# Kernel tuning notes

Hardware: AMD Instinct MI355X
Metric: run time of the kernel (lower is better)

Reference implementation:

```python
import jax, jax.numpy as jnp
import numpy as np
from functools import partial

D, H, W = 32, 256, 256   # grid_size (D, H, W)
V = 40000                # number of active voxels
C_IN, C_OUT = 16, 32
K = 3                    # kernel size
P = 32                   # max_points per voxel
EPS = 1e-5               # BatchNorm eps


def setup_inputs() -> dict:
    key = jax.random.key(0)
    k1, k2, k3, k4 = jax.random.split(key, 4)
    voxels = jax.random.normal(k1, (V, C_IN, P), dtype=jnp.float32)
    lin = jax.random.choice(k2, D * H * W, (V,), replace=False)
    d = (lin // (H * W)).astype(jnp.int32)
    h = ((lin // W) % H).astype(jnp.int32)
    w = (lin % W).astype(jnp.int32)
    indices = jnp.stack([w, h, d], axis=1)  # columns are (w, h, d) per original usage
    conv_w = jax.random.normal(k3, (C_OUT, C_IN, K, K, K), dtype=jnp.float32) * 0.05
    conv_b = jax.random.normal(k4, (C_OUT,), dtype=jnp.float32) * 0.05
    gamma = jnp.ones((C_OUT,), dtype=jnp.float32)
    beta = jnp.zeros((C_OUT,), dtype=jnp.float32)
    return {"voxels": voxels, "indices": indices, "conv_w": conv_w,
            "conv_b": conv_b, "gamma": gamma, "beta": beta, "batch_size": 1}


def reference(voxels, indices, conv_w, conv_b, gamma, beta, batch_size):
    # voxel features: mean over points  [V, C]
    feats = voxels.mean(axis=2)
    w_i, h_i, d_i = indices[:, 0], indices[:, 1], indices[:, 2]
    # original: batch_mask = indices[:,0] >= 0, plus per-dim bounds check
    valid = ((w_i >= 0) & (w_i < W) & (h_i >= 0) & (h_i < H) & (d_i >= 0) & (d_i < D))
    d_s = jnp.where(valid, d_i, D)  # route invalid rows out-of-bounds -> dropped
    # fused scatter replacing the python per-voxel loop; [D, H, W, C]
    grid = jnp.zeros((D, H, W, C_IN), dtype=voxels.dtype).at[d_s, h_i, w_i].set(
        feats, mode="drop")
    # same scatter is written into every batch slice in the original
    dense = jnp.broadcast_to(jnp.transpose(grid, (3, 0, 1, 2))[None],
                             (batch_size, C_IN, D, H, W))
    # Conv3d, padding = K//2 (SAME)
    out = jax.lax.conv_general_dilated(
        dense, conv_w, window_strides=(1, 1, 1), padding=[(K // 2, K // 2)] * 3,
        dimension_numbers=("NCDHW", "OIDHW", "NCDHW"))
    out = out + conv_b[None, :, None, None, None]
    # BatchNorm3d (training-mode batch statistics, biased variance)
    mean = out.mean(axis=(0, 2, 3, 4), keepdims=True)
    var = out.var(axis=(0, 2, 3, 4), keepdims=True)
    out = (out - mean) * jax.lax.rsqrt(var + EPS)
    out = out * gamma[None, :, None, None, None] + beta[None, :, None, None, None]
    return jax.nn.relu(out)
```

## Files before the change

kernel.cpp:

```cpp
#include <hip/hip_runtime.h>

#define D_   32
#define H_   256
#define W_   256
#define HW_  (H_ * W_)
#define DHW_ (D_ * H_ * W_)
#define V_   40000
#define CIN  16
#define COUT 32
#define P_   32
#define EPS_ 1e-5f

#define TD 2
#define TH 8
#define TW 32
#define NTX (W_ / TW)
#define NTY (H_ / TH)
#define NTZ (D_ / TD)
#define NT  (NTX * NTY * NTZ)
#define TPOS (TD * TH * TW)
#define OH 8
#define NQ (COUT / OH)
#define TROW 9
#define TCT 512
#define SSLOT 64
#define VBLK ((V_ + 255) / 256)
#define WTN  (NQ * 27 * 4 * OH)
#define WTBLK ((WTN + 255) / 256)

__global__ void tap_count_kernel(const int* __restrict__ idxs, int* __restrict__ tapcnt,
                                 const float* __restrict__ conv_w, float4* __restrict__ wt4) {
    int b = blockIdx.x;
    if (b >= VBLK) {
        int n = (b - VBLK) * 256 + threadIdx.x;
        if (n < WTN) {
            int oo = n & 7;
            int jj = (n >> 3) & 3;
            int m  = n >> 5;
            int k  = m % 27;
            int quarter = m / 27;
            int o = quarter * OH + oo;
            float4 wv;
            wv.x = conv_w[(o * CIN + 4 * jj + 0) * 27 + k];
            wv.y = conv_w[(o * CIN + 4 * jj + 1) * 27 + k];
            wv.z = conv_w[(o * CIN + 4 * jj + 2) * 27 + k];
            wv.w = conv_w[(o * CIN + 4 * jj + 3) * 27 + k];
            wt4[n] = wv;
        }
        return;
    }
    int v = b * 256 + threadIdx.x;
    if (v >= V_) return;
    int w = idxs[3 * v], h = idxs[3 * v + 1], d = idxs[3 * v + 2];
    if (!((unsigned)w < W_ && (unsigned)h < H_ && (unsigned)d < D_)) return;
    int dlo = max(d - 1, 0), dhi = min(d + 1, D_ - 1);
    int hlo = max(h - 1, 0), hhi = min(h + 1, H_ - 1);
    int wlo = max(w - 1, 0), whi = min(w + 1, W_ - 1);
    for (int tz = dlo / TD; tz <= dhi / TD; ++tz) {
        int zl = max(dlo, tz * TD), zh = min(dhi, tz * TD + TD - 1);
        for (int ty = hlo / TH; ty <= hhi / TH; ++ty) {
            int yl = max(hlo, ty * TH), yh = min(hhi, ty * TH + TH - 1);
            for (int tx = wlo / TW; tx <= whi / TW; ++tx) {
                int xl = max(wlo, tx * TW), xh = min(whi, tx * TW + TW - 1);
                int cnt = (zh - zl + 1) * (yh - yl + 1) * (xh - xl + 1);
                atomicAdd(&tapcnt[tz * NTY * NTX + ty * NTX + tx], cnt);
            }
        }
    }
}

__global__ void scan_kernel(const int* __restrict__ counts, int* __restrict__ starts,
                            int* __restrict__ cursor) {
    __shared__ int part[256];
    int t = threadIdx.x;
    int base = t * 16;
    int s = 0;
    for (int j = 0; j < 16; ++j) s += counts[base + j];
    part[t] = s;
    __syncthreads();
    for (int off = 1; off < 256; off <<= 1) {
        int val = part[t];
        int add = (t >= off) ? part[t - off] : 0;
        __syncthreads();
        part[t] = val + add;
        __syncthreads();
    }
    int run = (t > 0) ? part[t - 1] : 0;
    for (int j = 0; j < 16; ++j) {
        starts[base + j] = run;
        cursor[base + j] = run;
        run += counts[base + j];
    }
}

__global__ void tap_fill_kernel(const int* __restrict__ idxs, int* __restrict__ cursor,
                                int* __restrict__ tapbuf) {
    int v = blockIdx.x * 256 + threadIdx.x;
    if (v >= V_) return;
    int w = idxs[3 * v], h = idxs[3 * v + 1], d = idxs[3 * v + 2];
    if (!((unsigned)w < W_ && (unsigned)h < H_ && (unsigned)d < D_)) return;
    int dlo = max(d - 1, 0), dhi = min(d + 1, D_ - 1);
    int hlo = max(h - 1, 0), hhi = min(h + 1, H_ - 1);
    int wlo = max(w - 1, 0), whi = min(w + 1, W_ - 1);
    for (int tz = dlo / TD; tz <= dhi / TD; ++tz) {
        int zl = max(dlo, tz * TD), zh = min(dhi, tz * TD + TD - 1);
        for (int ty = hlo / TH; ty <= hhi / TH; ++ty) {
            int yl = max(hlo, ty * TH), yh = min(hhi, ty * TH + TH - 1);
            for (int tx = wlo / TW; tx <= whi / TW; ++tx) {
                int xl = max(wlo, tx * TW), xh = min(whi, tx * TW + TW - 1);
                int cnt = (zh - zl + 1) * (yh - yl + 1) * (xh - xl + 1);
                int p = atomicAdd(&cursor[tz * NTY * NTX + ty * NTX + tx], cnt);
                for (int dq = zl; dq <= zh; ++dq)
                    for (int hq = yl; hq <= yh; ++hq)
                        for (int wq = xl; wq <= xh; ++wq) {
                            int k = ((d - dq + 1) * 3 + (h - hq + 1)) * 3 + (w - wq + 1);
                            int pos = ((dq & (TD - 1)) * TH + (hq & (TH - 1))) * TW
                                    + (wq & (TW - 1));
                            tapbuf[p++] = (v << 14) | (k << 9) | pos;
                        }
            }
        }
    }
}

__global__ void featpack_kernel(const float* __restrict__ vox, float4* __restrict__ feats4) {
    int idx = blockIdx.x * 256 + threadIdx.x;
    if (idx >= V_ * 4) return;
    int v = idx >> 2, q = idx & 3;
    const float* base = vox + ((size_t)v * CIN + 4 * q) * P_;
    float m[4];
#pragma unroll
    for (int c = 0; c < 4; ++c) {
        const float4* p = (const float4*)(base + c * P_);
        float s = 0.f;
#pragma unroll
        for (int j = 0; j < P_ / 4; ++j) {
            float4 t = p[j];
            s += t.x + t.y + t.z + t.w;
        }
        m[c] = s * (1.0f / (float)P_);
    }
    feats4[v * 4 + q] = make_float4(m[0], m[1], m[2], m[3]);
}

__global__ void __launch_bounds__(TCT, 8) tile_conv_kernel(
    const float4* __restrict__ feats4, const float4* __restrict__ wt4,
    const int* __restrict__ tapstart, const int* __restrict__ tapcnt,
    const int* __restrict__ tapbuf, float* __restrict__ stats,
    float* __restrict__ out)
{
    __shared__ float  tile[TPOS * TROW];
    __shared__ float4 wsm4[27 * 4 * OH];
    __shared__ float  wsum[8][OH], wsq[8][OH];

    int t = threadIdx.x;
    int tile_id = blockIdx.x;
    int quarter = blockIdx.y;
    int gs = tapstart[tile_id];
    int nt = tapcnt[tile_id];
    int tx = tile_id % NTX, ty = (tile_id / NTX) % NTY, tz = tile_id / (NTX * NTY);
    int w0 = tx * TW, h0 = ty * TH, d0 = tz * TD;
    int obase = quarter * OH;

    for (int j = t; j < TPOS * TROW / 4; j += TCT)
        ((float4*)tile)[j] = make_float4(0, 0, 0, 0);
    for (int j = t; j < 27 * 4 * OH; j += TCT)
        wsm4[j] = wt4[quarter * (27 * 4 * OH) + j];
    __syncthreads();

    int oo = t & 7;
    int slot = t >> 3;
    int j = slot;
    if (j < nt) {
        unsigned tap = (unsigned)tapbuf[gs + j];
        const float4* fp = feats4 + (size_t)(tap >> 14) * 4;
        float4 f0 = fp[0], f1 = fp[1], f2 = fp[2], f3 = fp[3];
        while (true) {
            int jn = j + 64;
            bool more = jn < nt;
            unsigned tapn = 0u;
            float4 g0, g1, g2, g3;
            if (more) {
                tapn = (unsigned)tapbuf[gs + jn];
                const float4* gp = feats4 + (size_t)(tapn >> 14) * 4;
                g0 = gp[0]; g1 = gp[1]; g2 = gp[2]; g3 = gp[3];
            }
            int pos = tap & 511;
            int k = (tap >> 9) & 31;
            const float4* wp = &wsm4[(k * 4) * OH + oo];
            float4 q0 = wp[0], q1 = wp[8], q2 = wp[16], q3 = wp[24];
            float acc = q0.x * f0.x + q0.y * f0.y + q0.z * f0.z + q0.w * f0.w
                      + q1.x * f1.x + q1.y * f1.y + q1.z * f1.z + q1.w * f1.w
                      + q2.x * f2.x + q2.y * f2.y + q2.z * f2.z + q2.w * f2.w
                      + q3.x * f3.x + q3.y * f3.y + q3.z * f3.z + q3.w * f3.w;
            atomicAdd(&tile[pos * TROW + oo], acc);
            if (!more) break;
            tap = tapn; f0 = g0; f1 = g1; f2 = g2; f3 = g3; j = jn;
        }
    }
    __syncthreads();

    float s1 = 0.f, s2 = 0.f;
    for (int p = slot; p < TPOS; p += 64) {
        float sv = tile[p * TROW + oo];
        s1 += sv;
        s2 += sv * sv;
    }
    s1 += __shfl_xor(s1, 8);  s2 += __shfl_xor(s2, 8);
    s1 += __shfl_xor(s1, 16); s2 += __shfl_xor(s2, 16);
    s1 += __shfl_xor(s1, 32); s2 += __shfl_xor(s2, 32);
    int wave = t >> 6, lane = t & 63;
    if (lane < OH) { wsum[wave][lane] = s1; wsq[wave][lane] = s2; }

    int wl = t & 31;
    for (int r = t >> 5; r < OH * TD * TH; r += 16) {
        int oo2 = r >> 4;
        int rem = r & 15;
        int pos = rem * TW + wl;
        int dl = rem >> 3, hl = rem & 7;
        out[(size_t)(obase + oo2) * DHW_ + (size_t)(d0 + dl) * HW_ +
            (size_t)(h0 + hl) * W_ + (w0 + wl)] = tile[pos * TROW + oo2];
    }
    __syncthreads();
    if (t < OH) {
        float a = 0.f, b = 0.f;
#pragma unroll
        for (int wv = 0; wv < 8; ++wv) { a += wsum[wv][t]; b += wsq[wv][t]; }
        int sl = tile_id & (SSLOT - 1);
        atomicAdd(&stats[(obase + t) * SSLOT + sl], a);
        atomicAdd(&stats[COUT * SSLOT + (obase + t) * SSLOT + sl], b);
    }
}

__global__ void finalize_kernel(const float* __restrict__ stats,
                                const float* __restrict__ gamma,
                                const float* __restrict__ beta,
                                float* __restrict__ mi) {
    int t = threadIdx.x;
    if (t < COUT) {
        float m1 = 0.f, m2 = 0.f;
        for (int s = 0; s < SSLOT; ++s) {
            m1 += stats[t * SSLOT + s];
            m2 += stats[COUT * SSLOT + t * SSLOT + s];
        }
        float n = (float)DHW_;
        m1 /= n;
        m2 /= n;
        float var = fmaxf(m2 - m1 * m1, 0.f);
        float inv = rsqrtf(var + EPS_);
        float A = gamma[t] * inv;
        mi[t] = A;
        mi[COUT + t] = -m1 * A + beta[t];
    }
}

__global__ void norm_kernel(float* __restrict__ out, const float* __restrict__ mi) {
    int idx4 = blockIdx.x * 256 + threadIdx.x;
    int c = idx4 >> 19;
    float A = mi[c], B = mi[COUT + c];
    float4 x = ((const float4*)out)[idx4];
    x.x = fmaxf(x.x * A + B, 0.f);
    x.y = fmaxf(x.y * A + B, 0.f);
    x.z = fmaxf(x.z * A + B, 0.f);
    x.w = fmaxf(x.w * A + B, 0.f);
    ((float4*)out)[idx4] = x;
}

extern "C" void kernel_launch(void* const* d_in, const int* in_sizes, int n_in,
                              void* d_out, int out_size, void* d_ws, size_t ws_size,
                              hipStream_t stream) {
    const float* voxels  = (const float*)d_in[0];
    const int*   indices = (const int*)  d_in[1];
    const float* conv_w  = (const float*)d_in[2];
    const float* gamma   = (const float*)d_in[4];
    const float* beta    = (const float*)d_in[5];
    float* out = (float*)d_out;

    float4* wt4      = (float4*)d_ws;
    float*  stats    = (float*)(wt4 + WTN);
    float*  mi       = stats + 2 * COUT * SSLOT;
    int*    tapcnt   = (int*)(mi + 2 * COUT);
    int*    tapstart = tapcnt + NT;
    int*    tapcur   = tapstart + NT;
    float4* feats4   = (float4*)(tapcur + NT);
    int*    tapbuf   = (int*)(feats4 + (size_t)V_ * 4);

    hipMemsetAsync(tapcnt, 0, NT * sizeof(int), stream);
    hipMemsetAsync(stats, 0, 2 * COUT * SSLOT * sizeof(float), stream);

    tap_count_kernel<<<VBLK + WTBLK, 256, 0, stream>>>(indices, tapcnt, conv_w, wt4);
    scan_kernel<<<1, 256, 0, stream>>>(tapcnt, tapstart, tapcur);
    tap_fill_kernel<<<VBLK, 256, 0, stream>>>(indices, tapcur, tapbuf);
    featpack_kernel<<<(V_ * 4 + 255) / 256, 256, 0, stream>>>(voxels, feats4);

    dim3 grid(NT, NQ);
    tile_conv_kernel<<<grid, TCT, 0, stream>>>(feats4, wt4, tapstart, tapcnt, tapbuf,
                                               stats, out);
    finalize_kernel<<<1, 64, 0, stream>>>(stats, gamma, beta, mi);

    const int n4 = COUT * DHW_ / 4;
    norm_kernel<<<n4 / 256, 256, 0, stream>>>(out, mi);
}
```

Measured before the change: 664.0 us.

## Merge prep kernels, loop output quarters in-block, fuse finalize into norm

Folds tap counting, weight packing and feature averaging into one prep kernel. The stats zeroing moves into the scan kernel, and the BN finalize step is merged into the norm kernel, which cuts launch count. The conv kernel now loops over the four output-channel quarters inside one block and caches the tile's tap list in shared memory, so taps are not re-read per quarter. It also drops the software prefetch of the next tap, computes stats with per-wave shuffles during the output store, and adds more global atomics.

Result: slower. 811.4 us (+22.2%).

```diff
diff --git a/kernel.cpp b/kernel.cpp
--- a/kernel.cpp
+++ b/kernel.cpp
@@ -24,15 +24,41 @@
 #define TROW 9
 #define TCT 512
 #define SSLOT 64
+#define TAPC 640
 #define VBLK ((V_ + 255) / 256)
 #define WTN  (NQ * 27 * 4 * OH)
 #define WTBLK ((WTN + 255) / 256)
-
-__global__ void tap_count_kernel(const int* __restrict__ idxs, int* __restrict__ tapcnt,
-                                 const float* __restrict__ conv_w, float4* __restrict__ wt4) {
+#define FPBLK ((V_ * 4 + 255) / 256)
+
+__global__ void prep_kernel(const int* __restrict__ idxs, int* __restrict__ tapcnt,
+                            const float* __restrict__ conv_w, float4* __restrict__ wt4,
+                            const float* __restrict__ vox, float4* __restrict__ feats4) {
     int b = blockIdx.x;
-    if (b >= VBLK) {
-        int n = (b - VBLK) * 256 + threadIdx.x;
+    int t = threadIdx.x;
+    if (b < VBLK) {
+        int v = b * 256 + t;
+        if (v >= V_) return;
+        int w = idxs[3 * v], h = idxs[3 * v + 1], d = idxs[3 * v + 2];
+        if (!((unsigned)w < W_ && (unsigned)h < H_ && (unsigned)d < D_)) return;
+        int dlo = max(d - 1, 0), dhi = min(d + 1, D_ - 1);
+        int hlo = max(h - 1, 0), hhi = min(h + 1, H_ - 1);
+        int wlo = max(w - 1, 0), whi = min(w + 1, W_ - 1);
+        for (int tz = dlo / TD; tz <= dhi / TD; ++tz) {
+            int zl = max(dlo, tz * TD), zh = min(dhi, tz * TD + TD - 1);
+            for (int ty = hlo / TH; ty <= hhi / TH; ++ty) {
+                int yl = max(hlo, ty * TH), yh = min(hhi, ty * TH + TH - 1);
+                for (int tx = wlo / TW; tx <= whi / TW; ++tx) {
+                    int xl = max(wlo, tx * TW), xh = min(whi, tx * TW + TW - 1);
+                    int cnt = (zh - zl + 1) * (yh - yl + 1) * (xh - xl + 1);
+                    atomicAdd(&tapcnt[tz * NTY * NTX + ty * NTX + tx], cnt);
+                }
+            }
+        }
+        return;
+    }
+    b -= VBLK;
+    if (b < WTBLK) {
+        int n = b * 256 + t;
         if (n < WTN) {
             int oo = n & 7;
             int jj = (n >> 3) & 3;
@@ -49,30 +75,30 @@
         }
         return;
     }
-    int v = b * 256 + threadIdx.x;
-    if (v >= V_) return;
-    int w = idxs[3 * v], h = idxs[3 * v + 1], d = idxs[3 * v + 2];
-    if (!((unsigned)w < W_ && (unsigned)h < H_ && (unsigned)d < D_)) return;
-    int dlo = max(d - 1, 0), dhi = min(d + 1, D_ - 1);
-    int hlo = max(h - 1, 0), hhi = min(h + 1, H_ - 1);
-    int wlo = max(w - 1, 0), whi = min(w + 1, W_ - 1);
-    for (int tz = dlo / TD; tz <= dhi / TD; ++tz) {
-        int zl = max(dlo, tz * TD), zh = min(dhi, tz * TD + TD - 1);
-        for (int ty = hlo / TH; ty <= hhi / TH; ++ty) {
-            int yl = max(hlo, ty * TH), yh = min(hhi, ty * TH + TH - 1);
-            for (int tx = wlo / TW; tx <= whi / TW; ++tx) {
-                int xl = max(wlo, tx * TW), xh = min(whi, tx * TW + TW - 1);
-                int cnt = (zh - zl + 1) * (yh - yl + 1) * (xh - xl + 1);
-                atomicAdd(&tapcnt[tz * NTY * NTX + ty * NTX + tx], cnt);
-            }
-        }
-    }
+    b -= WTBLK;
+    int idx = b * 256 + t;
+    int v = idx >> 2, q = idx & 3;
+    const float* base = vox + ((size_t)v * CIN + 4 * q) * P_;
+    float m[4];
+#pragma unroll
+    for (int c = 0; c < 4; ++c) {
+        const float4* p = (const float4*)(base + c * P_);
+        float s = 0.f;
+#pragma unroll
+        for (int j = 0; j < P_ / 4; ++j) {
+            float4 tv = p[j];
+            s += tv.x + tv.y + tv.z + tv.w;
+        }
+        m[c] = s * (1.0f / (float)P_);
+    }
+    feats4[v * 4 + q] = make_float4(m[0], m[1], m[2], m[3]);
 }
 
 __global__ void scan_kernel(const int* __restrict__ counts, int* __restrict__ starts,
-                            int* __restrict__ cursor) {
+                            int* __restrict__ cursor, float* __restrict__ stats) {
     __shared__ int part[256];
     int t = threadIdx.x;
+    for (int j = t; j < 2 * COUT * SSLOT; j += 256) stats[j] = 0.f;
     int base = t * 16;
     int s = 0;
     for (int j = 0; j < 16; ++j) s += counts[base + j];
@@ -123,26 +149,6 @@
     }
 }
 
-__global__ void featpack_kernel(const float* __restrict__ vox, float4* __restrict__ feats4) {
-    int idx = blockIdx.x * 256 + threadIdx.x;
-    if (idx >= V_ * 4) return;
-    int v = idx >> 2, q = idx & 3;
-    const float* base = vox + ((size_t)v * CIN + 4 * q) * P_;
-    float m[4];
-#pragma unroll
-    for (int c = 0; c < 4; ++c) {
-        const float4* p = (const float4*)(base + c * P_);
-        float s = 0.f;
-#pragma unroll
-        for (int j = 0; j < P_ / 4; ++j) {
-            float4 t = p[j];
-            s += t.x + t.y + t.z + t.w;
-        }
-        m[c] = s * (1.0f / (float)P_);
-    }
-    feats4[v * 4 + q] = make_float4(m[0], m[1], m[2], m[3]);
-}
-
 __global__ void __launch_bounds__(TCT, 8) tile_conv_kernel(
     const float4* __restrict__ feats4, const float4* __restrict__ wt4,
     const int* __restrict__ tapstart, const int* __restrict__ tapcnt,
@@ -151,42 +157,40 @@
 {
     __shared__ float  tile[TPOS * TROW];
     __shared__ float4 wsm4[27 * 4 * OH];
-    __shared__ float  wsum[8][OH], wsq[8][OH];
+    __shared__ int    taps_l[TAPC];
 
     int t = threadIdx.x;
     int tile_id = blockIdx.x;
-    int quarter = blockIdx.y;
     int gs = tapstart[tile_id];
     int nt = tapcnt[tile_id];
     int tx = tile_id % NTX, ty = (tile_id / NTX) % NTY, tz = tile_id / (NTX * NTY);
     int w0 = tx * TW, h0 = ty * TH, d0 = tz * TD;
-    int obase = quarter * OH;
-
-    for (int j = t; j < TPOS * TROW / 4; j += TCT)
-        ((float4*)tile)[j] = make_float4(0, 0, 0, 0);
-    for (int j = t; j < 27 * 4 * OH; j += TCT)
-        wsm4[j] = wt4[quarter * (27 * 4 * OH) + j];
-    __syncthreads();
-
-    int oo = t & 7;
-    int slot = t >> 3;
-    int j = slot;
-    if (j < nt) {
-        unsigned tap = (unsigned)tapbuf[gs + j];
-        const float4* fp = feats4 + (size_t)(tap >> 14) * 4;
-        float4 f0 = fp[0], f1 = fp[1], f2 = fp[2], f3 = fp[3];
-        while (true) {
-            int jn = j + 64;
-            bool more = jn < nt;
-            unsigned tapn = 0u;
-            float4 g0, g1, g2, g3;
-            if (more) {
-                tapn = (unsigned)tapbuf[gs + jn];
-                const float4* gp = feats4 + (size_t)(tapn >> 14) * 4;
-                g0 = gp[0]; g1 = gp[1]; g2 = gp[2]; g3 = gp[3];
-            }
+    int sl = tile_id & (SSLOT - 1);
+
+    int ntl = min(nt, TAPC);
+    for (int j = t; j < ntl; j += TCT) taps_l[j] = tapbuf[gs + j];
+
+    int oo = t & 7, slot = t >> 3;
+    int wl = t & 31, rem = t >> 5;
+    size_t outb = (size_t)(d0 + (rem >> 3)) * HW_ + (size_t)(h0 + (rem & 7)) * W_
+                + (size_t)(w0 + wl);
+    int posD = (rem * TW + wl) * TROW;
+
+    for (int qq = 0; qq < NQ; ++qq) {
+        int obase = qq * OH;
+        for (int j = t; j < TPOS * TROW / 4; j += TCT)
+            ((float4*)tile)[j] = make_float4(0, 0, 0, 0);
+        for (int j = t; j < 27 * 4 * OH; j += TCT)
+            wsm4[j] = wt4[qq * (27 * 4 * OH) + j];
+        __syncthreads();
+
+        for (int j = slot; j < nt; j += 64) {
+            unsigned tap = (unsigned)((j < TAPC) ? taps_l[j] : tapbuf[gs + j]);
             int pos = tap & 511;
             int k = (tap >> 9) & 31;
+            int src = tap >> 14;
+            const float4* fp = feats4 + (size_t)src * 4;
+            float4 f0 = fp[0], f1 = fp[1], f2 = fp[2], f3 = fp[3];
             const float4* wp = &wsm4[(k * 4) * OH + oo];
             float4 q0 = wp[0], q1 = wp[8], q2 = wp[16], q3 = wp[24];
             float acc = q0.x * f0.x + q0.y * f0.y + q0.z * f0.z + q0.w * f0.w
@@ -194,76 +198,70 @@
                       + q2.x * f2.x + q2.y * f2.y + q2.z * f2.z + q2.w * f2.w
                       + q3.x * f3.x + q3.y * f3.y + q3.z * f3.z + q3.w * f3.w;
             atomicAdd(&tile[pos * TROW + oo], acc);
-            if (!more) break;
-            tap = tapn; f0 = g0; f1 = g1; f2 = g2; f3 = g3; j = jn;
+        }
+        __syncthreads();
+
+        for (int i = 0; i < OH; ++i) {
+            float v = tile[posD + i];
+            out[(size_t)(obase + i) * DHW_ + outb] = v;
+            float a = v, bb = v * v;
+            a += __shfl_xor(a, 1);  bb += __shfl_xor(bb, 1);
+            a += __shfl_xor(a, 2);  bb += __shfl_xor(bb, 2);
+            a += __shfl_xor(a, 4);  bb += __shfl_xor(bb, 4);
+            a += __shfl_xor(a, 8);  bb += __shfl_xor(bb, 8);
+            a += __shfl_xor(a, 16); bb += __shfl_xor(bb, 16);
+            a += __shfl_xor(a, 32); bb += __shfl_xor(bb, 32);
+            if ((t & 63) == 0) {
+                atomicAdd(&stats[(obase + i) * SSLOT + sl], a);
+                atomicAdd(&stats[COUT * SSLOT + (obase + i) * SSLOT + sl], bb);
+            }
+        }
+        __syncthreads();
+    }
+}
+
+__global__ void __launch_bounds__(256) norm_kernel(float* __restrict__ out,
+                                                   const float* __restrict__ stats,
+                                                   const float* __restrict__ gamma,
+                                                   const float* __restrict__ beta) {
+    __shared__ float sAB[2];
+    int t = threadIdx.x;
+    int bid = blockIdx.x;
+    int c = bid >> 7;
+    if (t < 64) {
+        float a = stats[c * SSLOT + t];
+        float b = stats[COUT * SSLOT + c * SSLOT + t];
+        a += __shfl_xor(a, 1);  b += __shfl_xor(b, 1);
+        a += __shfl_xor(a, 2);  b += __shfl_xor(b, 2);
+        a += __shfl_xor(a, 4);  b += __shfl_xor(b, 4);
+        a += __shfl_xor(a, 8);  b += __shfl_xor(b, 8);
+        a += __shfl_xor(a, 16); b += __shfl_xor(b, 16);
+        a += __shfl_xor(a, 32); b += __shfl_xor(b, 32);
+        if (t == 0) {
+            float n = (float)DHW_;
+            float m1 = a / n, m2 = b / n;
+            float var = fmaxf(m2 - m1 * m1, 0.f);
+            float inv = rsqrtf(var + EPS_);
+            float A = gamma[c] * inv;
+            sAB[0] = A;
+            sAB[1] = -m1 * A + beta[c];
         }
     }
     __syncthreads();
-
-    float s1 = 0.f, s2 = 0.f;
-    for (int p = slot; p < TPOS; p += 64) {
-        float sv = tile[p * TROW + oo];
-        s1 += sv;
-        s2 += sv * sv;
-    }
-    s1 += __shfl_xor(s1, 8);  s2 += __shfl_xor(s2, 8);
-    s1 += __shfl_xor(s1, 16); s2 += __shfl_xor(s2, 16);
-    s1 += __shfl_xor(s1, 32); s2 += __shfl_xor(s2, 32);
-    int wave = t >> 6, lane = t & 63;
-    if (lane < OH) { wsum[wave][lane] = s1; wsq[wave][lane] = s2; }
-
-    int wl = t & 31;
-    for (int r = t >> 5; r < OH * TD * TH; r += 16) {
-        int oo2 = r >> 4;
-        int rem = r & 15;
-        int pos = rem * TW + wl;
-        int dl = rem >> 3, hl = rem & 7;
-        out[(size_t)(obase + oo2) * DHW_ + (size_t)(d0 + dl) * HW_ +
-            (size_t)(h0 + hl) * W_ + (w0 + wl)] = tile[pos * TROW + oo2];
-    }
-    __syncthreads();
-    if (t < OH) {
-        float a = 0.f, b = 0.f;
+    float A = sAB[0], B = sAB[1];
+    const int CH4 = DHW_ / 4;
+    int base4 = c * CH4 + (bid & 127) * (CH4 / 128);
+    float4* o4 = (float4*)out;
 #pragma unroll
-        for (int wv = 0; wv < 8; ++wv) { a += wsum[wv][t]; b += wsq[wv][t]; }
-        int sl = tile_id & (SSLOT - 1);
-        atomicAdd(&stats[(obase + t) * SSLOT + sl], a);
-        atomicAdd(&stats[COUT * SSLOT + (obase + t) * SSLOT + sl], b);
-    }
-}
-
-__global__ void finalize_kernel(const float* __restrict__ stats,
-                                const float* __restrict__ gamma,
-                                const float* __restrict__ beta,
-                                float* __restrict__ mi) {
-    int t = threadIdx.x;
-    if (t < COUT) {
-        float m1 = 0.f, m2 = 0.f;
-        for (int s = 0; s < SSLOT; ++s) {
-            m1 += stats[t * SSLOT + s];
-            m2 += stats[COUT * SSLOT + t * SSLOT + s];
-        }
-        float n = (float)DHW_;
-        m1 /= n;
-        m2 /= n;
-        float var = fmaxf(m2 - m1 * m1, 0.f);
-        float inv = rsqrtf(var + EPS_);
-        float A = gamma[t] * inv;
-        mi[t] = A;
-        mi[COUT + t] = -m1 * A + beta[t];
-    }
-}
-
-__global__ void norm_kernel(float* __restrict__ out, const float* __restrict__ mi) {
-    int idx4 = blockIdx.x * 256 + threadIdx.x;
-    int c = idx4 >> 19;
-    float A = mi[c], B = mi[COUT + c];
-    float4 x = ((const float4*)out)[idx4];
-    x.x = fmaxf(x.x * A + B, 0.f);
-    x.y = fmaxf(x.y * A + B, 0.f);
-    x.z = fmaxf(x.z * A + B, 0.f);
-    x.w = fmaxf(x.w * A + B, 0.f);
-    ((float4*)out)[idx4] = x;
+    for (int i = 0; i < 16; ++i) {
+        int idx4 = base4 + i * 256 + t;
+        float4 x = o4[idx4];
+        x.x = fmaxf(x.x * A + B, 0.f);
+        x.y = fmaxf(x.y * A + B, 0.f);
+        x.z = fmaxf(x.z * A + B, 0.f);
+        x.w = fmaxf(x.w * A + B, 0.f);
+        o4[idx4] = x;
+    }
 }
 
 extern "C" void kernel_launch(void* const* d_in, const int* in_sizes, int n_in,
@@ -284,20 +282,17 @@
     int*    tapcur   = tapstart + NT;
     float4* feats4   = (float4*)(tapcur + NT);
     int*    tapbuf   = (int*)(feats4 + (size_t)V_ * 4);
+    (void)mi;
 
     hipMemsetAsync(tapcnt, 0, NT * sizeof(int), stream);
-    hipMemsetAsync(stats, 0, 2 * COUT * SSLOT * sizeof(float), stream);
-
-    tap_count_kernel<<<VBLK + WTBLK, 256, 0, stream>>>(indices, tapcnt, conv_w, wt4);
-    scan_kernel<<<1, 256, 0, stream>>>(tapcnt, tapstart, tapcur);
+
+    prep_kernel<<<VBLK + WTBLK + FPBLK, 256, 0, stream>>>(indices, tapcnt, conv_w, wt4,
+                                                          voxels, feats4);
+    scan_kernel<<<1, 256, 0, stream>>>(tapcnt, tapstart, tapcur, stats);
     tap_fill_kernel<<<VBLK, 256, 0, stream>>>(indices, tapcur, tapbuf);
-    featpack_kernel<<<(V_ * 4 + 255) / 256, 256, 0, stream>>>(voxels, feats4);
-
-    dim3 grid(NT, NQ);
-    tile_conv_kernel<<<grid, TCT, 0, stream>>>(feats4, wt4, tapstart, tapcnt, tapbuf,
-                                               stats, out);
-    finalize_kernel<<<1, 64, 0, stream>>>(stats, gamma, beta, mi);
-
-    const int n4 = COUT * DHW_ / 4;
-    norm_kernel<<<n4 / 256, 256, 0, stream>>>(out, mi);
-}
+
+    tile_conv_kernel<<<NT, TCT, 0, stream>>>(feats4, wt4, tapstart, tapcnt, tapbuf,
+                                             stats, out);
+
+    norm_kernel<<<COUT * 128, 256, 0, stream>>>(out, stats, gamma, beta);
+}
```
